# Optimization experiments

Hardware: AMD Instinct MI355X
Metric: run time of the kernel (lower is better)

## Reference

```python
import jax, jax.numpy as jnp
import numpy as np

# skimage uniform LBP (P=8, R=1) sample offsets: rr = -R*sin(2*pi*p/P), cc = R*cos(2*pi*p/P),
# rounded to 5 decimals as in skimage, with bilinear interpolation and cval=0 outside the image.
_P = 8
_OFFS = [(round(float(-np.sin(2.0 * np.pi * p / _P)), 5), round(float(np.cos(2.0 * np.pi * p / _P)), 5)) for p in range(_P)]


def _uniform_lbp(gray):
    """gray: [B, F, H, W] quantized float (0..255). Returns normalized uniform LBP, same shape."""
    B, F, H, W = gray.shape
    pad = jnp.pad(gray, ((0, 0), (0, 0), (1, 1), (1, 1)))  # zeros outside, matching skimage cval=0

    def shift(dr, dc):  # integer shift via slicing of the padded frame stack
        return pad[:, :, 1 + dr:1 + dr + H, 1 + dc:1 + dc + W]

    def sample(dr, dc):  # bilinear interpolation at fractional offset (dr, dc)
        r0, c0 = int(np.floor(dr)), int(np.floor(dc))
        fr, fc = dr - r0, dc - c0
        if fr < 1e-7 and fc < 1e-7:
            return shift(r0, c0)
        return ((1.0 - fr) * (1.0 - fc)) * shift(r0, c0) \
             + ((1.0 - fr) * fc) * shift(r0, c0 + 1) \
             + (fr * (1.0 - fc)) * shift(r0 + 1, c0) \
             + (fr * fc) * shift(r0 + 1, c0 + 1)

    bits = [(sample(dr, dc) >= gray) for (dr, dc) in _OFFS]
    ones = jnp.zeros(gray.shape, jnp.float32)
    changes = jnp.zeros(gray.shape, jnp.int32)
    for p in range(_P):
        ones = ones + bits[p].astype(jnp.float32)
        changes = changes + (bits[p] ^ bits[(p + 1) % _P]).astype(jnp.int32)
    lbp = jnp.where(changes <= 2, ones, jnp.float32(_P + 1))  # 'uniform' method: codes 0..9
    # per-frame normalization: lbp /= lbp.max() when max > 0
    m = lbp.max(axis=(2, 3), keepdims=True)
    return jnp.where(m > 0, lbp / jnp.maximum(m, 1.0), lbp)


def _conv3d(x, w, b, stride):
    y = jax.lax.conv_general_dilated(
        x, w, window_strides=stride, padding=[(1, 1)] * 3,
        dimension_numbers=("NCDHW", "OIDHW", "NCDHW"))
    return y + b[None, :, None, None, None]


def _enhanced_3d_cnn(lbp3, w1, b1, w2, b2):
    h = jax.nn.relu(_conv3d(lbp3, w1, b1, (1, 2, 2)))   # [B,64,F,H/2,W/2]
    h = jax.nn.relu(_conv3d(h, w2, b2, (2, 2, 2)))      # [B,128,F/2,H/4,W/4]
    return h.mean(axis=(2, 3, 4))                        # [B,128] global avg pool


def setup_inputs() -> dict:
    key = jax.random.key(0)
    k1, k2, k3 = jax.random.split(key, 3)
    x = jax.random.uniform(k1, (4, 3, 16, 224, 224), jnp.float32)
    w1 = jax.random.normal(k2, (64, 3, 3, 3, 3), jnp.float32) * 0.05
    b1 = jnp.zeros((64,), jnp.float32)
    w2 = jax.random.normal(k3, (128, 64, 3, 3, 3), jnp.float32) * 0.05
    b2 = jnp.zeros((128,), jnp.float32)
    return {"x": x, "w1": w1, "b1": b1, "w2": w2, "b2": b2}


def reference(x, w1, b1, w2, b2):
    B, C, F, H, W = x.shape
    gray = jnp.floor(x.mean(axis=1) * 255.0)         # == (gray*255).astype(uint8) for x in [0,1]
    lbp = _uniform_lbp(gray)                          # [B,F,H,W]
    lbp3 = jnp.broadcast_to(lbp[:, None], (B, 3, F, H, W))
    return _enhanced_3d_cnn(lbp3, w1, b1, w2, b2)     # [B,128]
```

## Files before the change

### kernel.cpp

```cpp
#include <hip/hip_runtime.h>
#include <hip/hip_bf16.h>
#include <stdint.h>

constexpr int NB = 4;
constexpr int NF = 16;
constexpr int NH = 224, NW = 224;
constexpr int HWPIX = NH * NW;
constexpr int OC2 = 128;

typedef __attribute__((ext_vector_type(8))) __bf16 bf16x8;
typedef __attribute__((ext_vector_type(4))) float f32x4;

#define MFMA16(a, b, c) __builtin_amdgcn_mfma_f32_16x16x32_bf16(a, b, c, 0, 0, 0)

__device__ __forceinline__ ushort bf16u(float f) {
  __hip_bfloat16 h = __float2bfloat16(f);
  return *(ushort*)&h;
}

__global__ __launch_bounds__(256) void graylbp_kernel(const float* __restrict__ x,
                                                      unsigned char* __restrict__ lbpc,
                                                      int* __restrict__ blockmax) {
  __shared__ float sg[18 * 18];
  const int tile = blockIdx.x;
  const int frame = blockIdx.y;
  const int ty = tile / 14, tx = tile - ty * 14;
  const int b = frame >> 4, f = frame & 15;
  const float* xb = x + ((size_t)b * 3 * NF + f) * HWPIX;

  for (int e = threadIdx.x; e < 324; e += 256) {
    int r = e / 18, cc = e - 18 * r;
    int y = ty * 16 + r - 1, xx = tx * 16 + cc - 1;
    float v = 0.0f;
    if ((unsigned)y < (unsigned)NH && (unsigned)xx < (unsigned)NW) {
      size_t o = (size_t)y * NW + xx;
      float s = xb[o] + xb[o + (size_t)NF * HWPIX] + xb[o + 2 * (size_t)NF * HWPIX];
      v = floorf((s / 3.0f) * 255.0f);
    }
    sg[e] = v;
  }
  __syncthreads();

  const int r = threadIdx.x >> 4, cc = threadIdx.x & 15;
  float n[3][3];
#pragma unroll
  for (int dy = 0; dy < 3; ++dy)
#pragma unroll
    for (int dx = 0; dx < 3; ++dx) n[dy][dx] = sg[(r + dy) * 18 + (cc + dx)];
  float c = n[1][1];

  constexpr double Ad = 0.70711;
  constexpr double Bd = 1.0 - Ad;

  const float s0 = n[1][2];
  const float s2 = n[0][1];
  const float s4 = n[1][0];
  const float s6 = n[2][1];
  const float s1 = (float)(Ad * Bd) * n[0][1] + (float)(Ad * Ad) * n[0][2]
                 + (float)(Bd * Bd) * n[1][1] + (float)(Bd * Ad) * n[1][2];
  const float s3 = (float)(Ad * Ad) * n[0][0] + (float)(Ad * Bd) * n[0][1]
                 + (float)(Bd * Ad) * n[1][0] + (float)(Bd * Bd) * n[1][1];
  const float s5 = (float)(Bd * Ad) * n[1][0] + (float)(Bd * Bd) * n[1][1]
                 + (float)(Ad * Ad) * n[2][0] + (float)(Ad * Bd) * n[2][1];
  const float s7 = (float)(Bd * Bd) * n[1][1] + (float)(Bd * Ad) * n[1][2]
                 + (float)(Ad * Bd) * n[2][1] + (float)(Ad * Ad) * n[2][2];

  bool bb[8] = { s0 >= c, s1 >= c, s2 >= c, s3 >= c,
                 s4 >= c, s5 >= c, s6 >= c, s7 >= c };
  int ones = 0, changes = 0;
#pragma unroll
  for (int p = 0; p < 8; ++p) {
    ones += bb[p] ? 1 : 0;
    changes += (bb[p] != bb[(p + 1) & 7]) ? 1 : 0;
  }
  int code = (changes <= 2) ? ones : 9;
  lbpc[(size_t)frame * HWPIX + (ty * 16 + r) * NW + tx * 16 + cc] = (unsigned char)code;

  int m = code;
#pragma unroll
  for (int off = 32; off >= 1; off >>= 1) m = max(m, __shfl_down(m, off, 64));
  __shared__ int wm[4];
  if ((threadIdx.x & 63) == 0) wm[threadIdx.x >> 6] = m;
  __syncthreads();
  if (threadIdx.x == 0)
    blockmax[frame * 196 + tile] = max(max(wm[0], wm[1]), max(wm[2], wm[3]));
}

__global__ void framemax_tab_kernel(const int* __restrict__ blockmax,
                                    __hip_bfloat16* __restrict__ normtab) {
  int t = threadIdx.x;
  int f = t >> 2, part = t & 3;
  int m = 0;
  for (int j = part; j < 196; j += 4) m = max(m, blockmax[f * 196 + j]);
  m = max(m, __shfl_xor(m, 1, 64));
  m = max(m, __shfl_xor(m, 2, 64));
  if (part == 0) {
    for (int cde = 0; cde < 16; ++cde) {
      float v = (m > 0) ? ((float)cde / (float)m) : (float)cde;
      normtab[f * 16 + cde] = __float2bfloat16(v);
    }
  }
}

__global__ void w1r_kernel(const float* __restrict__ w1, const float* __restrict__ b1,
                           __hip_bfloat16* __restrict__ w1r) {
  int o = threadIdx.x;
  if (o >= 64) return;
  for (int k = 0; k < 32; ++k) {
    float v;
    if (k < 27)      v = w1[o * 81 + k] + w1[o * 81 + 27 + k] + w1[o * 81 + 54 + k];
    else if (k == 27) v = b1[o];
    else              v = 0.0f;
    w1r[o * 32 + k] = __float2bfloat16(v);
  }
}

__global__ __launch_bounds__(256) void w2r_kernel(const float* __restrict__ w2,
                                                  __hip_bfloat16* __restrict__ w2r) {
  int i = blockIdx.x * 256 + threadIdx.x;
  if (i >= 27 * 128 * 64) return;
  int tap = i / (128 * 64);
  int rem = i - tap * (128 * 64);
  int oc = rem >> 6, ic = rem & 63;
  w2r[i] = __float2bfloat16(w2[((size_t)oc * 64 + ic) * 27 + tap]);
}

constexpr int ROWB2 = 57 * 256;
constexpr int LSTR = 232;
constexpr int LT_TASKS = 3 * 11 * 58;

__global__ __launch_bounds__(256, 2) void fused_conv(
    const unsigned char* __restrict__ lbpc,
    const __hip_bfloat16* __restrict__ normtab,
    const __hip_bfloat16* __restrict__ w1r,
    const __hip_bfloat16* __restrict__ w2r,
    const float* __restrict__ b2,
    float* __restrict__ partial) {
  __shared__ __align__(16) char slab[5 * ROWB2];
  __shared__ __align__(4) unsigned char ltile[3 * 11 * LSTR];
  __shared__ ushort stabL[80];

  const int gg = blockIdx.x;
  const int f2 = blockIdx.y;
  const int b = blockIdx.z;
  const int tid = threadIdx.x;
  const int lane = tid & 63, w = tid >> 6;
  const int c = lane & 15, q = lane >> 4;
  const int oc0 = w * 32;
  const f32x4 zero4 = {0.f, 0.f, 0.f, 0.f};

  if (tid < 80) {
    int u = tid >> 4, cde = tid & 15;
    int fin = 2 * f2 - 2 + u;
    stabL[tid] = ((unsigned)fin < (unsigned)NF)
        ? ((const ushort*)normtab)[(b * NF + fin) * 16 + cde] : (ushort)0;
  }

  int x2v[7], rb2[7];
#pragma unroll
  for (int j = 0; j < 7; ++j) {
    int pos = j * 16 + c;
    int yo = pos >= 56 ? 1 : 0;
    x2v[j] = pos - 56 * yo;
    rb2[j] = yo * 2 * ROWB2 + x2v[j] * 256;
  }

  bf16x8 afr[4];
  const __bf16* w1rb = (const __bf16*)w1r;
#pragma unroll
  for (int ocg = 0; ocg < 4; ++ocg)
    afr[ocg] = *(const bf16x8*)(w1rb + ((ocg * 16 + c) << 5) + q * 8);

  int pre[8], se[8]; bool vld[8]; ushort fbv[8];
#pragma unroll
  for (int e = 0; e < 8; ++e) {
    int k = q * 8 + e;
    vld[e] = (k < 27);
    fbv[e] = (k == 27) ? (ushort)0x3F80 : (ushort)0;
    int kk = vld[e] ? k : 0;
    int kfc = kk / 9, r9 = kk - 9 * kfc;
    int ky = r9 / 3, kx = r9 - 3 * ky;
    pre[e] = (kfc * 11 + ky) * LSTR + 4 + (2 * c - 1 + kx);
    se[e] = kfc * 16;
  }

  float bias[2][4];
#pragma unroll
  for (int i = 0; i < 2; ++i)
#pragma unroll
    for (int r = 0; r < 4; ++r) bias[i][r] = b2[oc0 + i * 16 + q * 4 + r];

  f32x4 acc[2][7];
#pragma unroll
  for (int i = 0; i < 2; ++i)
#pragma unroll
    for (int j = 0; j < 7; ++j) acc[i][j] = zero4;

  const __bf16* w2rb = (const __bf16*)w2r;

  if (tid < 40) {
    int r = tid >> 3, u = tid & 7;
    *(int4*)(slab + r * ROWB2 + (u >> 2) * 128 + (u & 3) * 16) = make_int4(0, 0, 0, 0);
  }

  auto FILL = [&](int kf) {
    const int f1 = 2 * f2 - 1 + kf;
    for (int idx = tid; idx < LT_TASKS; idx += 256) {
      int kfc = idx / 638, rem = idx - kfc * 638;
      int row = rem / 58, chunk = rem - row * 58;
      uint32_t v = 0;
      if (chunk >= 1 && chunk <= 56) {
        int fin = f1 - 1 + kfc, yin = 8 * gg - 3 + row;
        if ((unsigned)fin < (unsigned)NF && (unsigned)yin < (unsigned)NH)
          v = *(const uint32_t*)(lbpc + (size_t)(b * NF + fin) * HWPIX + yin * NW + (chunk - 1) * 4);
      }
      *(uint32_t*)(ltile + (kfc * 11 + row) * LSTR + chunk * 4) = v;
    }
  };

  auto CONV1 = [&](int kf) {
    const int f1 = 2 * f2 - 1 + kf;
    if ((unsigned)f1 >= (unsigned)NF) return;
    const int koff = kf * 16;
    for (int fi = w; fi < 35; fi += 4) {
      int rr = fi / 7, fx = fi - 7 * rr;
      int y1 = 4 * gg - 1 + rr;
      int xs = fx * 16 + c + 1;
      int t = xs >> 1, k7 = t & 7, sub = xs & 1;
      char* wbase = slab + rr * ROWB2 + t * 256 + (q & 1) * 8;
      if ((unsigned)y1 < 112u) {
        union { bf16x8 v; ushort u[8]; } bu;
        int foff = rr * (2 * LSTR) + fx * 32;
#pragma unroll
        for (int e = 0; e < 8; ++e) {
          int code = ltile[pre[e] + foff];
          bu.u[e] = vld[e] ? stabL[koff + se[e] + code] : fbv[e];
        }
#pragma unroll
        for (int ocg = 0; ocg < 4; ++ocg) {
          f32x4 a = MFMA16(afr[ocg], bu.v, zero4);
          ushort4 o;
          o.x = bf16u(fmaxf(a[0], 0.0f));
          o.y = bf16u(fmaxf(a[1], 0.0f));
          o.z = bf16u(fmaxf(a[2], 0.0f));
          o.w = bf16u(fmaxf(a[3], 0.0f));
          int ich = ocg >> 1;
          int g8 = sub * 4 + (ocg & 1) * 2 + (q >> 1);
          *(ushort4*)(wbase + ich * 128 + ((g8 ^ k7) << 4)) = o;
        }
      } else {
        ushort4 z; z.x = z.y = z.z = z.w = 0;
#pragma unroll
        for (int ocg = 0; ocg < 4; ++ocg) {
          int ich = ocg >> 1;
          int g8 = sub * 4 + (ocg & 1) * 2 + (q >> 1);
          *(ushort4*)(wbase + ich * 128 + ((g8 ^ k7) << 4)) = z;
        }
      }
    }
  };

  FILL(0);
  __syncthreads();
  CONV1(0);

  for (int kf = 0; kf < 3; ++kf) {
    __syncthreads();
    const int f1 = 2 * f2 - 1 + kf;
    const bool fok = (unsigned)f1 < (unsigned)NF;

    uint32_t fv[8];
    if (kf < 2) {
      const int f1n = f1 + 1;
#pragma unroll
      for (int i = 0; i < 8; ++i) {
        int idx = tid + i * 256;
        uint32_t v = 0;
        if (idx < LT_TASKS) {
          int kfc = idx / 638, rem = idx - kfc * 638;
          int row = rem / 58, chunk = rem - row * 58;
          if (chunk >= 1 && chunk <= 56) {
            int fin = f1n - 1 + kfc, yin = 8 * gg - 3 + row;
            if ((unsigned)fin < (unsigned)NF && (unsigned)yin < (unsigned)NH)
              v = *(const uint32_t*)(lbpc + (size_t)(b * NF + fin) * HWPIX + yin * NW + (chunk - 1) * 4);
          }
        }
        fv[i] = v;
      }
    }

    if (fok) {
#pragma unroll
      for (int ky = 0; ky < 3; ++ky) {
#pragma unroll
        for (int kx = 0; kx < 3; ++kx) {
          const int tap = kf * 9 + ky * 3 + kx;
          const int sx = kx >> 1;
          const int sb4 = (kx & 1) * 4 + q;
          const int immr = ky * ROWB2 + sx * 256;
#pragma unroll
          for (int ich = 0; ich < 2; ++ich) {
            const __bf16* wtap = w2rb + (((size_t)tap * 128 + oc0 + c) << 6)
                               + ich * 32 + q * 8;
            bf16x8 a0 = *(const bf16x8*)(wtap);
            bf16x8 a1 = *(const bf16x8*)(wtap + (16 << 6));
#pragma unroll
            for (int j = 0; j < 7; ++j) {
              int slot = sb4 ^ ((x2v[j] + sx) & 7);
              bf16x8 bv = *(const bf16x8*)(slab + rb2[j] + immr + ich * 128 + (slot << 4));
              acc[0][j] = MFMA16(a0, bv, acc[0][j]);
              acc[1][j] = MFMA16(a1, bv, acc[1][j]);
            }
          }
        }
      }
    }

    if (kf < 2) {
#pragma unroll
      for (int i = 0; i < 8; ++i) {
        int idx = tid + i * 256;
        if (idx < LT_TASKS) {
          int kfc = idx / 638, rem = idx - kfc * 638;
          int row = rem / 58, chunk = rem - row * 58;
          *(uint32_t*)(ltile + (kfc * 11 + row) * LSTR + chunk * 4) = fv[i];
        }
      }
    }
    __syncthreads();
    if (kf < 2) CONV1(kf + 1);
  }

#pragma unroll
  for (int i = 0; i < 2; ++i) {
#pragma unroll
    for (int r = 0; r < 4; ++r) {
      float s = 0.0f;
#pragma unroll
      for (int j = 0; j < 7; ++j) s += fmaxf(acc[i][j][r] + bias[i][r], 0.0f);
      s += __shfl_xor(s, 1);
      s += __shfl_xor(s, 2);
      s += __shfl_xor(s, 4);
      s += __shfl_xor(s, 8);
      if (c == 0) {
        int oc = oc0 + i * 16 + q * 4 + r;
        partial[((size_t)b * OC2 + oc) * 224 + f2 * 28 + gg] = s;
      }
    }
  }
}

__global__ void final_kernel(const float* __restrict__ partial, float* __restrict__ out) {
  int i = blockIdx.x * 256 + threadIdx.x;
  float s = 0.0f;
  for (int j = 0; j < 224; ++j) s += partial[(size_t)i * 224 + j];
  out[i] = s / 25088.0f;
}

extern "C" void kernel_launch(void* const* d_in, const int* in_sizes, int n_in,
                              void* d_out, int out_size, void* d_ws, size_t ws_size,
                              hipStream_t stream) {
  const float* x  = (const float*)d_in[0];
  const float* w1 = (const float*)d_in[1];
  const float* b1 = (const float*)d_in[2];
  const float* w2 = (const float*)d_in[3];
  const float* b2 = (const float*)d_in[4];
  float* out = (float*)d_out;

  char* ws = (char*)d_ws;
  unsigned char* lbpc = (unsigned char*)ws;
  int* blockmax = (int*)(ws + 3211264);
  __hip_bfloat16* normtab = (__hip_bfloat16*)(ws + 3261440);
  float* partial = (float*)(ws + 3263488);
  __hip_bfloat16* w2r = (__hip_bfloat16*)(ws + 3722240);
  __hip_bfloat16* w1r = (__hip_bfloat16*)(ws + 4164608);

  w1r_kernel<<<1, 64, 0, stream>>>(w1, b1, w1r);
  w2r_kernel<<<(27 * 128 * 64 + 255) / 256, 256, 0, stream>>>(w2, w2r);
  graylbp_kernel<<<dim3(196, NB * NF), 256, 0, stream>>>(x, lbpc, blockmax);
  framemax_tab_kernel<<<1, 256, 0, stream>>>(blockmax, normtab);
  fused_conv<<<dim3(28, 8, 4), 256, 0, stream>>>(lbpc, normtab, w1r, w2r, b2, partial);
  final_kernel<<<2, 256, 0, stream>>>(partial, out);
}
```

Measured before the change: 135.1 us.

## Pre-normalize LBP to bf16 and load conv1 operands directly from global

Adds a separate kernel that turns LBP codes into normalized bf16 values per frame. The fused conv then builds its conv1 MFMA operands by loading row segments straight from global memory, split across two MFMAs with reorganized weight matrices. This removes the LDS ltile staging, the lookup table and their prefetch and sync logic. It also remaps block indices with a swizzle over a 1D grid. The trade-off is an extra pass that writes a bf16 array twice the size of the byte codes, plus more global traffic and an extra MFMA inside conv1.

```diff
diff --git a/kernel.cpp b/kernel.cpp
--- a/kernel.cpp
+++ b/kernel.cpp
@@ -6,6 +6,7 @@
 constexpr int NF = 16;
 constexpr int NH = 224, NW = 224;
 constexpr int HWPIX = NH * NW;
+constexpr int NPIX = NB * NF * HWPIX;
 constexpr int OC2 = 128;
 
 typedef __attribute__((ext_vector_type(8))) __bf16 bf16x8;
@@ -102,16 +103,38 @@
   }
 }
 
-__global__ void w1r_kernel(const float* __restrict__ w1, const float* __restrict__ b1,
-                           __hip_bfloat16* __restrict__ w1r) {
+__global__ __launch_bounds__(256) void normlbp_kernel(const unsigned char* __restrict__ lbpc,
+                                                      const __hip_bfloat16* __restrict__ normtab,
+                                                      __hip_bfloat16* __restrict__ lbpn) {
+  int i = blockIdx.x * 256 + threadIdx.x;
+  int frame = (i * 8) / HWPIX;
+  const ushort* tab = (const ushort*)normtab + frame * 16;
+  uint2 cds = *(const uint2*)(lbpc + (size_t)i * 8);
+  uint o0 = (uint)tab[cds.x & 0xFF] | ((uint)tab[(cds.x >> 8) & 0xFF] << 16);
+  uint o1 = (uint)tab[(cds.x >> 16) & 0xFF] | ((uint)tab[cds.x >> 24] << 16);
+  uint o2 = (uint)tab[cds.y & 0xFF] | ((uint)tab[(cds.y >> 8) & 0xFF] << 16);
+  uint o3 = (uint)tab[(cds.y >> 16) & 0xFF] | ((uint)tab[cds.y >> 24] << 16);
+  uint4 ov; ov.x = o0; ov.y = o1; ov.z = o2; ov.w = o3;
+  *(uint4*)((ushort*)lbpn + (size_t)i * 8) = ov;
+}
+
+__global__ void w1m_kernel(const float* __restrict__ w1, const float* __restrict__ b1,
+                           __hip_bfloat16* __restrict__ w1m1,
+                           __hip_bfloat16* __restrict__ w1m2) {
   int o = threadIdx.x;
   if (o >= 64) return;
+  float wsum[27];
+  for (int t = 0; t < 27; ++t)
+    wsum[t] = w1[o * 81 + t] + w1[o * 81 + 27 + t] + w1[o * 81 + 54 + t];
   for (int k = 0; k < 32; ++k) {
-    float v;
-    if (k < 27)      v = w1[o * 81 + k] + w1[o * 81 + 27 + k] + w1[o * 81 + 54 + k];
-    else if (k == 27) v = b1[o];
-    else              v = 0.0f;
-    w1r[o * 32 + k] = __float2bfloat16(v);
+    int r = k >> 2, el = k & 3;
+    float v1 = 0.0f, v2 = 0.0f;
+    if (r < 3 && el >= 1) v1 = wsum[r * 3 + el - 1];
+    if (r == 3 && el == 0) v1 = b1[o];
+    if (r >= 4 && r < 7 && el >= 1) v1 = wsum[9 + (r - 4) * 3 + el - 1];
+    if (r < 3 && el >= 1) v2 = wsum[18 + r * 3 + el - 1];
+    w1m1[o * 32 + k] = __float2bfloat16(v1);
+    w1m2[o * 32 + k] = __float2bfloat16(v2);
   }
 }
 
@@ -126,36 +149,29 @@
 }
 
 constexpr int ROWB2 = 57 * 256;
-constexpr int LSTR = 232;
-constexpr int LT_TASKS = 3 * 11 * 58;
 
 __global__ __launch_bounds__(256, 2) void fused_conv(
-    const unsigned char* __restrict__ lbpc,
-    const __hip_bfloat16* __restrict__ normtab,
-    const __hip_bfloat16* __restrict__ w1r,
+    const __hip_bfloat16* __restrict__ lbpn,
+    const __hip_bfloat16* __restrict__ w1m1,
+    const __hip_bfloat16* __restrict__ w1m2,
     const __hip_bfloat16* __restrict__ w2r,
     const float* __restrict__ b2,
     float* __restrict__ partial) {
   __shared__ __align__(16) char slab[5 * ROWB2];
-  __shared__ __align__(4) unsigned char ltile[3 * 11 * LSTR];
-  __shared__ ushort stabL[80];
-
-  const int gg = blockIdx.x;
-  const int f2 = blockIdx.y;
-  const int b = blockIdx.z;
+
+  const int wg = blockIdx.x;
+  const int swz = (wg & 7) * 112 + (wg >> 3);
+  const int gg = swz % 28;
+  const int rem = swz / 28;
+  const int f2 = rem & 7;
+  const int b = rem >> 3;
+
   const int tid = threadIdx.x;
   const int lane = tid & 63, w = tid >> 6;
   const int c = lane & 15, q = lane >> 4;
   const int oc0 = w * 32;
   const f32x4 zero4 = {0.f, 0.f, 0.f, 0.f};
 
-  if (tid < 80) {
-    int u = tid >> 4, cde = tid & 15;
-    int fin = 2 * f2 - 2 + u;
-    stabL[tid] = ((unsigned)fin < (unsigned)NF)
-        ? ((const ushort*)normtab)[(b * NF + fin) * 16 + cde] : (ushort)0;
-  }
-
   int x2v[7], rb2[7];
 #pragma unroll
   for (int j = 0; j < 7; ++j) {
@@ -165,24 +181,22 @@
     rb2[j] = yo * 2 * ROWB2 + x2v[j] * 256;
   }
 
-  bf16x8 afr[4];
-  const __bf16* w1rb = (const __bf16*)w1r;
-#pragma unroll
-  for (int ocg = 0; ocg < 4; ++ocg)
-    afr[ocg] = *(const bf16x8*)(w1rb + ((ocg * 16 + c) << 5) + q * 8);
-
-  int pre[8], se[8]; bool vld[8]; ushort fbv[8];
-#pragma unroll
-  for (int e = 0; e < 8; ++e) {
-    int k = q * 8 + e;
-    vld[e] = (k < 27);
-    fbv[e] = (k == 27) ? (ushort)0x3F80 : (ushort)0;
-    int kk = vld[e] ? k : 0;
-    int kfc = kk / 9, r9 = kk - 9 * kfc;
-    int ky = r9 / 3, kx = r9 - 3 * ky;
-    pre[e] = (kfc * 11 + ky) * LSTR + 4 + (2 * c - 1 + kx);
-    se[e] = kfc * 16;
-  }
+  bf16x8 am1[4], am2[4];
+  const __bf16* w1m1b = (const __bf16*)w1m1;
+  const __bf16* w1m2b = (const __bf16*)w1m2;
+#pragma unroll
+  for (int ocg = 0; ocg < 4; ++ocg) {
+    am1[ocg] = *(const bf16x8*)(w1m1b + ((ocg * 16 + c) << 5) + q * 8);
+    am2[ocg] = *(const bf16x8*)(w1m2b + ((ocg * 16 + c) << 5) + q * 8);
+  }
+
+  const int rid0 = 2 * q - (q >> 1);
+  const int rid1 = rid0 + 1;
+  const bool use1 = (q == 0) || (q == 2);
+  const int rid2 = (q == 0) ? 6 : 8;
+  const bool use2 = (q <= 1);
+  const bool use3 = (q == 0);
+  const bool biasl = (q == 1);
 
   float bias[2][4];
 #pragma unroll
@@ -197,31 +211,29 @@
     for (int j = 0; j < 7; ++j) acc[i][j] = zero4;
 
   const __bf16* w2rb = (const __bf16*)w2r;
+  const char* lbpnb = (const char*)lbpn;
 
   if (tid < 40) {
     int r = tid >> 3, u = tid & 7;
     *(int4*)(slab + r * ROWB2 + (u >> 2) * 128 + (u & 3) * 16) = make_int4(0, 0, 0, 0);
   }
 
-  auto FILL = [&](int kf) {
-    const int f1 = 2 * f2 - 1 + kf;
-    for (int idx = tid; idx < LT_TASKS; idx += 256) {
-      int kfc = idx / 638, rem = idx - kfc * 638;
-      int row = rem / 58, chunk = rem - row * 58;
-      uint32_t v = 0;
-      if (chunk >= 1 && chunk <= 56) {
-        int fin = f1 - 1 + kfc, yin = 8 * gg - 3 + row;
-        if ((unsigned)fin < (unsigned)NF && (unsigned)yin < (unsigned)NH)
-          v = *(const uint32_t*)(lbpc + (size_t)(b * NF + fin) * HWPIX + yin * NW + (chunk - 1) * 4);
-      }
-      *(uint32_t*)(ltile + (kfc * 11 + row) * LSTR + chunk * 4) = v;
-    }
+  auto rowld = [&](int f1, int rid, bool use, int y1, long xb, uint& lo, uint& hi) {
+    int kfc = (rid >= 6) ? 2 : (rid >= 3 ? 1 : 0);
+    int ky = rid - kfc * 3;
+    int fin = f1 - 1 + kfc;
+    int yin = 2 * y1 - 1 + ky;
+    bool ok = use && ((unsigned)fin < (unsigned)NF) && ((unsigned)yin < (unsigned)NH);
+    long off = ok ? (((long)(b * NF + fin) * HWPIX + (long)yin * NW) * 2 + xb) : 0;
+    uint l = *(const uint*)(lbpnb + off);
+    uint h = *(const uint*)(lbpnb + off + 4);
+    lo = ok ? l : 0u;
+    hi = ok ? h : 0u;
   };
 
   auto CONV1 = [&](int kf) {
     const int f1 = 2 * f2 - 1 + kf;
     if ((unsigned)f1 >= (unsigned)NF) return;
-    const int koff = kf * 16;
     for (int fi = w; fi < 35; fi += 4) {
       int rr = fi / 7, fx = fi - 7 * rr;
       int y1 = 4 * gg - 1 + rr;
@@ -229,16 +241,24 @@
       int t = xs >> 1, k7 = t & 7, sub = xs & 1;
       char* wbase = slab + rr * ROWB2 + t * 256 + (q & 1) * 8;
       if ((unsigned)y1 < 112u) {
-        union { bf16x8 v; ushort u[8]; } bu;
-        int foff = rr * (2 * LSTR) + fx * 32;
-#pragma unroll
-        for (int e = 0; e < 8; ++e) {
-          int code = ltile[pre[e] + foff];
-          bu.u[e] = vld[e] ? stabL[koff + se[e] + code] : fbv[e];
+        const int x1 = fx * 16 + c;
+        const long xb = (long)(4 * x1 - 4);
+        uint r0l, r0h, r1l, r1h, r2l, r2h, r3l, r3h;
+        rowld(f1, rid0, true, y1, xb, r0l, r0h);
+        rowld(f1, rid1, use1, y1, xb, r1l, r1h);
+        rowld(f1, rid2, use2, y1, xb, r2l, r2h);
+        rowld(f1, 7,    use3, y1, xb, r3l, r3h);
+        if (x1 == 0) {
+          r0l &= 0xFFFFu; r1l &= 0xFFFFu; r2l &= 0xFFFFu; r3l &= 0xFFFFu;
         }
+        if (biasl) { r1l = 0x3F80u; r1h = 0u; }
+        union U8 { bf16x8 v; uint u[4]; } b1u, b2u;
+        b1u.u[0] = r0l; b1u.u[1] = r0h; b1u.u[2] = r1l; b1u.u[3] = r1h;
+        b2u.u[0] = r2l; b2u.u[1] = r2h; b2u.u[2] = r3l; b2u.u[3] = r3h;
 #pragma unroll
         for (int ocg = 0; ocg < 4; ++ocg) {
-          f32x4 a = MFMA16(afr[ocg], bu.v, zero4);
+          f32x4 a = MFMA16(am1[ocg], b1u.v, zero4);
+          a = MFMA16(am2[ocg], b2u.v, a);
           ushort4 o;
           o.x = bf16u(fmaxf(a[0], 0.0f));
           o.y = bf16u(fmaxf(a[1], 0.0f));
@@ -260,34 +280,12 @@
     }
   };
 
-  FILL(0);
-  __syncthreads();
   CONV1(0);
 
   for (int kf = 0; kf < 3; ++kf) {
     __syncthreads();
     const int f1 = 2 * f2 - 1 + kf;
     const bool fok = (unsigned)f1 < (unsigned)NF;
-
-    uint32_t fv[8];
-    if (kf < 2) {
-      const int f1n = f1 + 1;
-#pragma unroll
-      for (int i = 0; i < 8; ++i) {
-        int idx = tid + i * 256;
-        uint32_t v = 0;
-        if (idx < LT_TASKS) {
-          int kfc = idx / 638, rem = idx - kfc * 638;
-          int row = rem / 58, chunk = rem - row * 58;
-          if (chunk >= 1 && chunk <= 56) {
-            int fin = f1n - 1 + kfc, yin = 8 * gg - 3 + row;
-            if ((unsigned)fin < (unsigned)NF && (unsigned)yin < (unsigned)NH)
-              v = *(const uint32_t*)(lbpc + (size_t)(b * NF + fin) * HWPIX + yin * NW + (chunk - 1) * 4);
-          }
-        }
-        fv[i] = v;
-      }
-    }
 
     if (fok) {
 #pragma unroll
@@ -316,17 +314,6 @@
       }
     }
 
-    if (kf < 2) {
-#pragma unroll
-      for (int i = 0; i < 8; ++i) {
-        int idx = tid + i * 256;
-        if (idx < LT_TASKS) {
-          int kfc = idx / 638, rem = idx - kfc * 638;
-          int row = rem / 58, chunk = rem - row * 58;
-          *(uint32_t*)(ltile + (kfc * 11 + row) * LSTR + chunk * 4) = fv[i];
-        }
-      }
-    }
     __syncthreads();
     if (kf < 2) CONV1(kf + 1);
   }
@@ -373,12 +360,15 @@
   __hip_bfloat16* normtab = (__hip_bfloat16*)(ws + 3261440);
   float* partial = (float*)(ws + 3263488);
   __hip_bfloat16* w2r = (__hip_bfloat16*)(ws + 3722240);
-  __hip_bfloat16* w1r = (__hip_bfloat16*)(ws + 4164608);
-
-  w1r_kernel<<<1, 64, 0, stream>>>(w1, b1, w1r);
+  __hip_bfloat16* w1m1 = (__hip_bfloat16*)(ws + 4164608);
+  __hip_bfloat16* w1m2 = (__hip_bfloat16*)(ws + 4168704);
+  __hip_bfloat16* lbpn = (__hip_bfloat16*)(ws + 4172800);
+
+  w1m_kernel<<<1, 64, 0, stream>>>(w1, b1, w1m1, w1m2);
   w2r_kernel<<<(27 * 128 * 64 + 255) / 256, 256, 0, stream>>>(w2, w2r);
   graylbp_kernel<<<dim3(196, NB * NF), 256, 0, stream>>>(x, lbpc, blockmax);
   framemax_tab_kernel<<<1, 256, 0, stream>>>(blockmax, normtab);
-  fused_conv<<<dim3(28, 8, 4), 256, 0, stream>>>(lbpc, normtab, w1r, w2r, b2, partial);
+  normlbp_kernel<<<NPIX / 8 / 256, 256, 0, stream>>>(lbpc, normtab, lbpn);
+  fused_conv<<<896, 256, 0, stream>>>(lbpn, w1m1, w1m2, w2r, b2, partial);
   final_kernel<<<2, 256, 0, stream>>>(partial, out);
 }
```

After: 135.4 us. No clear change (+0.2%).
